# Optimization experiments

Hardware: AMD Instinct MI355X
Metric: run time of the kernel (lower is better)

The kernel has to match this reference:

```python
import jax, jax.numpy as jnp
import numpy as np

INF = 1e20


def setup_inputs() -> dict:
    key = jax.random.key(0)
    k0, k1, k2, k3, k4 = jax.random.split(key, 5)
    B, T, C, D = 4, 8, 512, 256
    P, Ks = 4, 4
    return {
        "context": jax.random.normal(k0, (B, T, C, D), jnp.float32),
        "ctx_mask": jax.random.randint(k1, (B, C), 0, 2).astype(jnp.int32),
        "weight_tensor": jax.random.normal(k2, (P, D), jnp.float32),
        "mean_dis": jax.random.uniform(k3, (Ks, 1), jnp.float32),
        "precision_inv_dis": jax.random.uniform(k4, (Ks, 1), jnp.float32),
        "topk": 10,
        "max_position_distance": 160,
    }


def _forward(context, ctx_mask, weight_tensor, mean_dis, precision_inv_dis, topk, max_position_distance):
    B, T, C, D = context.shape
    Ks = mean_dis.shape[0]
    # attention[b,t,c,e] = mean_p sum_d ctx[b,t,c,d]*relu(W[p,d])*ctx[b,t,e,d]
    # (mean over perspectives commutes with the contraction over d)
    wbar = jnp.mean(jax.nn.relu(weight_tensor), axis=0)  # (D,)
    attention = jnp.einsum('btcd,bted->btce', context * wbar, context)  # (B,T,C,C)

    valid = ctx_mask > 0  # (B,C)
    pair_ok = valid[:, None, :, None] & valid[:, None, None, :]  # (B,1,C,C)
    attention = jnp.where(pair_ok, attention, -INF)

    # spatial Gaussian kernels over |i-j| distances (shared across batch/turn)
    idx = jnp.arange(C)
    pc = jnp.abs(idx[:, None] - idx[None, :]).astype(jnp.float32)
    pc = jnp.minimum(pc, float(max_position_distance)) / float(max_position_distance)  # (C,C)
    mu = mean_dis[:, 0][:, None, None]            # (Ks,1,1)
    prec = precision_inv_dis[:, 0][:, None, None]  # (Ks,1,1)
    spatial = jnp.exp(-0.5 * (pc[None] - mu) ** 2 * prec ** 2)  # (Ks,C,C)

    # kNN sparsification
    knn_val, knn_ind = jax.lax.top_k(attention, topk)  # (B,T,C,K)
    sem = jax.nn.softmax(knn_val, axis=-1)             # semantic weights (B,T,C,K)

    idx5 = jnp.broadcast_to(knn_ind[:, :, None, :, :], (B, T, Ks, C, topk))
    spatial_full = jnp.broadcast_to(spatial[None, None], (B, T, Ks, C, C))
    sp_chosen = jnp.take_along_axis(spatial_full, idx5, axis=-1)  # (B,T,Ks,C,K)
    sp_chosen = sp_chosen / jnp.sum(sp_chosen, axis=-1, keepdims=True)

    attn_chosen = sem[:, :, None, :, :] * sp_chosen  # (B,T,Ks,C,K)

    adj = jnp.zeros((B, T, Ks, C, C), dtype=attn_chosen.dtype)
    adj = adj.at[
        jnp.arange(B)[:, None, None, None, None],
        jnp.arange(T)[None, :, None, None, None],
        jnp.arange(Ks)[None, None, :, None, None],
        jnp.arange(C)[None, None, None, :, None],
        idx5,
    ].set(attn_chosen)
    return adj


def reference(context, ctx_mask, weight_tensor, mean_dis, precision_inv_dis, topk, max_position_distance):
    return _forward(context, ctx_mask, weight_tensor, mean_dis, precision_inv_dis, topk, max_position_distance)
```

## Files before the change

kernel.cpp:

```cpp
#include <hip/hip_runtime.h>
#include <math.h>

#define C_ 512
#define D_ 256
#define KS_ 4
#define TOPK_ 10
#define NEG 1e20f

typedef float v2f __attribute__((ext_vector_type(2)));
typedef float v4f __attribute__((ext_vector_type(4)));

__device__ __forceinline__ int csw2(int g) { return g ^ ((g >> 3) & 1); }

#define ASTR 36
#define ASTR3 68
#define BSTR2 260
#define ABUF3 (16 * ASTR3)
#define BBUF3 (16 * BSTR2)

#define BARRIER_LDS() asm volatile("s_waitcnt lgkmcnt(0)\n\ts_barrier" ::: "memory")

#define PKFMA_LO(ACC, AP, BP) \
    asm("v_pk_fma_f32 %0, %1, %2, %0 op_sel:[0,0,0] op_sel_hi:[0,1,1]" \
        : "+v"(ACC) : "v"(AP), "v"(BP));
#define PKFMA_HI(ACC, AP, BP) \
    asm("v_pk_fma_f32 %0, %1, %2, %0 op_sel:[1,0,0] op_sel_hi:[1,1,1]" \
        : "+v"(ACC) : "v"(AP), "v"(BP));

extern "C" __global__ __launch_bounds__(256, 2)
void gemm_attn(const float* __restrict__ ctx,
               const float* __restrict__ W,
               float* __restrict__ ws,
               float* __restrict__ out)
{
    __shared__ __align__(16) float wbar_s[D_];
    __shared__ __align__(16) float a_s[2 * ABUF3];
    __shared__ __align__(16) float b_s[2 * BBUF3];

    const int tid  = threadIdx.x;
    const int lane = tid & 63;
    const int wv   = tid >> 6;
    const int wr   = (wv >> 1) * 32;
    const int wc   = (wv & 1) * 128;
    const int rg   = lane >> 4;
    const int cg   = lane & 15;

    const int blk  = blockIdx.x;
    const int bt   = (blk & 7) * 4 + ((blk >> 3) & 3);
    const int tile = blk >> 5;
    const int c0   = (tile & 7) * 64;
    const int n0   = (tile >> 3) * 256;

    const float* ctx_bt = ctx + (size_t)bt * (C_ * D_);
    float* zbase = out + (size_t)blk * 65536 + (size_t)tid * 4;

    {
        float w0 = W[tid], w1 = W[D_ + tid], w2 = W[2 * D_ + tid], w3 = W[3 * D_ + tid];
        wbar_s[tid] = 0.25f * (fmaxf(w0, 0.f) + fmaxf(w1, 0.f) + fmaxf(w2, 0.f) + fmaxf(w3, 0.f));
    }

    const int bcol = tid >> 2;
    const int bq   = tid & 3;
    const float* bsrc = ctx_bt + (size_t)(n0 + bcol) * D_ + bq * 4;
    const int bwoff = (4 * bq) * BSTR2 + bcol;
    const int ar_ = tid >> 2;
    const int aq  = tid & 3;
    const float* asrc = ctx_bt + (size_t)(c0 + ar_) * D_ + aq * 4;
    const int awoff = (4 * aq) * ASTR3 + ar_;
    const int abase = wr + rg * 8;
    const int bbase = wc + cg * 4;

    BARRIER_LDS();

    {
        v4f B0 = *(const v4f*)(bsrc + (size_t)0 * 64 * D_);
        v4f B1 = *(const v4f*)(bsrc + (size_t)1 * 64 * D_);
        v4f B2 = *(const v4f*)(bsrc + (size_t)2 * 64 * D_);
        v4f B3 = *(const v4f*)(bsrc + (size_t)3 * 64 * D_);
        v4f A0 = *(const v4f*)asrc;
        #pragma unroll
        for (int j = 0; j < 4; ++j) {
            b_s[bwoff + j * BSTR2 + 0 * 64] = B0[j];
            b_s[bwoff + j * BSTR2 + 1 * 64] = B1[j];
            b_s[bwoff + j * BSTR2 + 2 * 64] = B2[j];
            b_s[bwoff + j * BSTR2 + 3 * 64] = B3[j];
        }
        v4f wb = *(const v4f*)(wbar_s + aq * 4);
        a_s[awoff + 0 * ASTR3] = A0[0] * wb[0];
        a_s[awoff + 1 * ASTR3] = A0[1] * wb[1];
        a_s[awoff + 2 * ASTR3] = A0[2] * wb[2];
        a_s[awoff + 3 * ASTR3] = A0[3] * wb[3];
    }
    BARRIER_LDS();

    v2f acc2[8][4];
    #pragma unroll
    for (int j = 0; j < 8; ++j)
        #pragma unroll
        for (int t = 0; t < 4; ++t) acc2[j][t] = (v2f){0.f, 0.f};

    #define FMA_RANGE(K0, K1)                                                 \
        _Pragma("unroll")                                                     \
        for (int kk = (K0); kk < (K1); ++kk) {                                \
            v4f av0 = *(const v4f*)(acur + kk * ASTR3 + abase);               \
            v4f av1 = *(const v4f*)(acur + kk * ASTR3 + abase + 4);           \
            v4f bv0 = *(const v4f*)(bcur + kk * BSTR2 + bbase);               \
            v4f bv1 = *(const v4f*)(bcur + kk * BSTR2 + bbase + 64);          \
            v2f a01 = __builtin_shufflevector(av0, av0, 0, 1);                \
            v2f a23 = __builtin_shufflevector(av0, av0, 2, 3);                \
            v2f a45 = __builtin_shufflevector(av1, av1, 0, 1);                \
            v2f a67 = __builtin_shufflevector(av1, av1, 2, 3);                \
            v2f b0l = __builtin_shufflevector(bv0, bv0, 0, 1);                \
            v2f b0h = __builtin_shufflevector(bv0, bv0, 2, 3);                \
            v2f b1l = __builtin_shufflevector(bv1, bv1, 0, 1);                \
            v2f b1h = __builtin_shufflevector(bv1, bv1, 2, 3);                \
            PKFMA_LO(acc2[0][0], a01, b0l) PKFMA_LO(acc2[0][1], a01, b0h)     \
            PKFMA_LO(acc2[0][2], a01, b1l) PKFMA_LO(acc2[0][3], a01, b1h)     \
            PKFMA_HI(acc2[1][0], a01, b0l) PKFMA_HI(acc2[1][1], a01, b0h)     \
            PKFMA_HI(acc2[1][2], a01, b1l) PKFMA_HI(acc2[1][3], a01, b1h)     \
            PKFMA_LO(acc2[2][0], a23, b0l) PKFMA_LO(acc2[2][1], a23, b0h)     \
            PKFMA_LO(acc2[2][2], a23, b1l) PKFMA_LO(acc2[2][3], a23, b1h)     \
            PKFMA_HI(acc2[3][0], a23, b0l) PKFMA_HI(acc2[3][1], a23, b0h)     \
            PKFMA_HI(acc2[3][2], a23, b1l) PKFMA_HI(acc2[3][3], a23, b1h)     \
            PKFMA_LO(acc2[4][0], a45, b0l) PKFMA_LO(acc2[4][1], a45, b0h)     \
            PKFMA_LO(acc2[4][2], a45, b1l) PKFMA_LO(acc2[4][3], a45, b1h)     \
            PKFMA_HI(acc2[5][0], a45, b0l) PKFMA_HI(acc2[5][1], a45, b0h)     \
            PKFMA_HI(acc2[5][2], a45, b1l) PKFMA_HI(acc2[5][3], a45, b1h)     \
            PKFMA_LO(acc2[6][0], a67, b0l) PKFMA_LO(acc2[6][1], a67, b0h)     \
            PKFMA_LO(acc2[6][2], a67, b1l) PKFMA_LO(acc2[6][3], a67, b1h)     \
            PKFMA_HI(acc2[7][0], a67, b0l) PKFMA_HI(acc2[7][1], a67, b0h)     \
            PKFMA_HI(acc2[7][2], a67, b1l) PKFMA_HI(acc2[7][3], a67, b1h)     \
        }

    const v4f zv = (v4f){0.f, 0.f, 0.f, 0.f};

    for (int kt = 0; kt < 16; ++kt) {
        const float* acur = a_s + (kt & 1) * ABUF3;
        const float* bcur = b_s + (kt & 1) * BBUF3;
        float* anx = a_s + ((kt & 1) ^ 1) * ABUF3;
        float* bnx = b_s + ((kt & 1) ^ 1) * BBUF3;
        const bool pf = (kt < 15);

        v4f B0, B1, B2, B3, A0;
        if (pf) {
            const float* nb = bsrc + (kt + 1) * 16;
            B0 = *(const v4f*)(nb + (size_t)0 * 64 * D_);
            B1 = *(const v4f*)(nb + (size_t)1 * 64 * D_);
            B2 = *(const v4f*)(nb + (size_t)2 * 64 * D_);
            B3 = *(const v4f*)(nb + (size_t)3 * 64 * D_);
            A0 = *(const v4f*)(asrc + (kt + 1) * 16);
        }
        #pragma unroll
        for (int q = 0; q < 4; ++q)
            *(v4f*)(zbase + (size_t)(kt * 4 + q) * 1024) = zv;

        FMA_RANGE(0, 10)
        if (pf) {
            #pragma unroll
            for (int j = 0; j < 4; ++j) {
                bnx[bwoff + j * BSTR2 + 0 * 64] = B0[j];
                bnx[bwoff + j * BSTR2 + 1 * 64] = B1[j];
                bnx[bwoff + j * BSTR2 + 2 * 64] = B2[j];
                bnx[bwoff + j * BSTR2 + 3 * 64] = B3[j];
            }
            v4f wb = *(const v4f*)(wbar_s + (kt + 1) * 16 + aq * 4);
            anx[awoff + 0 * ASTR3] = A0[0] * wb[0];
            anx[awoff + 1 * ASTR3] = A0[1] * wb[1];
            anx[awoff + 2 * ASTR3] = A0[2] * wb[2];
            anx[awoff + 3 * ASTR3] = A0[3] * wb[3];
        }
        FMA_RANGE(10, 16)
        BARRIER_LDS();
    }
    #undef FMA_RANGE

    #pragma unroll
    for (int j = 0; j < 8; ++j) {
        float* wrow = ws + ((size_t)bt * C_ + c0 + wr + rg * 8 + j) * C_ + n0;
        v4f o0 = __builtin_shufflevector(acc2[j][0], acc2[j][1], 0, 1, 2, 3);
        v4f o1 = __builtin_shufflevector(acc2[j][2], acc2[j][3], 0, 1, 2, 3);
        *(v4f*)(wrow + bbase)      = o0;
        *(v4f*)(wrow + bbase + 64) = o1;
    }
}

extern "C" __global__ __launch_bounds__(256, 2)
void epilogue_k(const float* __restrict__ ws,
                const int* __restrict__ cmask,
                const float* __restrict__ mu_g,
                const float* __restrict__ pr_g,
                float* __restrict__ out)
{
    const int tid  = threadIdx.x;
    const int lane = tid & 63;
    const int wv   = tid >> 6;

    const int blk = blockIdx.x;
    const int bt  = blk >> 7;
    const int rq  = blk & 127;
    const int b   = bt >> 3;

    const int c  = rq * 4 + wv;
    const int vr = cmask[b * C_ + c];

    float row[8];
    {
        const float* wrow = ws + ((size_t)bt * C_ + c) * C_ + lane * 8;
        float4 r0 = *(const float4*)wrow;
        float4 r1 = *(const float4*)(wrow + 4);
        row[0] = r0.x; row[1] = r0.y; row[2] = r0.z; row[3] = r0.w;
        row[4] = r1.x; row[5] = r1.y; row[6] = r1.z; row[7] = r1.w;
        int4 m0 = *(const int4*)(cmask + b * C_ + lane * 8);
        int4 m1 = *(const int4*)(cmask + b * C_ + lane * 8 + 4);
        int em[8] = {m0.x, m0.y, m0.z, m0.w, m1.x, m1.y, m1.z, m1.w};
        #pragma unroll
        for (int i = 0; i < 8; ++i) {
            bool ok = (vr > 0) && (em[i] > 0);
            row[i] = ok ? row[i] : -NEG;
        }
    }

    float tv[TOPK_];
    int   te[TOPK_];
    unsigned int taken = 0;
    #pragma unroll
    for (int j = 0; j < TOPK_; ++j) {
        float lv = -3.3e38f;
        int   li = 0;
        #pragma unroll
        for (int i = 0; i < 8; ++i) {
            bool better = (!((taken >> i) & 1u)) && (row[i] > lv);
            lv = better ? row[i] : lv;
            li = better ? i : li;
        }
        int le = lane * 8 + li;
        #pragma unroll
        for (int off = 1; off < 64; off <<= 1) {
            float ov = __shfl_xor(lv, off);
            int   oe = __shfl_xor(le, off);
            bool take = (ov > lv) || (ov == lv && oe < le);
            lv = take ? ov : lv;
            le = take ? oe : le;
        }
        tv[j] = lv;
        te[j] = le;
        if ((le >> 3) == lane) taken |= 1u << (le & 7);
    }
    const float mx = tv[0];
    float ssum = 0.f;
    #pragma unroll
    for (int j = 0; j < TOPK_; ++j) ssum += expf(tv[j] - mx);

    if (lane < 40) {
        const int ksq = lane / 10;
        const int myj = lane - ksq * 10;
        const float mu = mu_g[ksq];
        const float pr = pr_g[ksq];
        float sps = 0.f, spj = 0.f, tvj = 0.f;
        int ej = 0;
        #pragma unroll
        for (int j = 0; j < TOPK_; ++j) {
            float d = fabsf((float)(te[j] - c));
            d = fminf(d, 160.f) * (1.0f / 160.0f);
            float x  = d - mu;
            float sp = expf(-0.5f * x * x * pr * pr);
            sps += sp;
            if (j == myj) { spj = sp; tvj = tv[j]; ej = te[j]; }
        }
        float oval = (expf(tvj - mx) / ssum) * (spj / sps);
        out[((size_t)(bt * KS_ + ksq) * C_ + c) * C_ + ej] = oval;
    }
}

#define BSTR 516
extern "C" __global__ __launch_bounds__(256, 2)
void graph_learner(const float* __restrict__ ctx,
                   const int* __restrict__ cmask,
                   const float* __restrict__ W,
                   const float* __restrict__ mu_g,
                   const float* __restrict__ pr_g,
                   float* __restrict__ out)
{
    __shared__ __align__(16) float wbar_s[D_];
    __shared__ __align__(16) float a_s[16 * ASTR];
    __shared__ __align__(16) float b_s[16 * BSTR];
    __shared__ __align__(8)  float res_s[2560];
    __shared__ unsigned int vmask_s[16];

    const int tid  = threadIdx.x;
    const int lane = tid & 63;
    const int wv   = tid >> 6;
    const int w8   = wv * 8;

    const int blk = blockIdx.x;
    const int bt  = (blk & 7) * 4 + ((blk >> 3) & 3);
    const int c0  = (blk >> 5) * 32;
    const int b   = bt >> 3;

    const float* ctx_bt = ctx + (size_t)bt * (C_ * D_);
    const int*   mask_b = cmask + b * C_;

    {
        float w0 = W[tid], w1 = W[D_ + tid], w2 = W[2 * D_ + tid], w3 = W[3 * D_ + tid];
        wbar_s[tid] = 0.25f * (fmaxf(w0, 0.f) + fmaxf(w1, 0.f) + fmaxf(w2, 0.f) + fmaxf(w3, 0.f));
    }
    if (tid < 16) {
        unsigned int m = 0;
        for (int i = 0; i < 32; ++i)
            m |= (mask_b[tid * 32 + i] > 0 ? 1u : 0u) << i;
        vmask_s[tid] = m;
    }

    const int brow = tid >> 2;
    const int bq   = tid & 3;
    const float* bsrc = ctx_bt + (size_t)brow * D_ + bq * 4;
    const int bwbase = (4 * bq) * BSTR + 4 * csw2(brow >> 2) + (brow & 3);
    const int ar_ = tid >> 2;
    const int aq  = tid & 3;
    const float* asrc = ctx_bt + (size_t)(c0 + ar_) * D_ + aq * 4;
    const int awbase = (4 * aq) * ASTR + ar_;
    const int bc0 = 4 * csw2(2 * lane);
    const int bc1 = 4 * csw2(2 * lane + 1);

    v2f acc2[8][4];
    #pragma unroll
    for (int j = 0; j < 8; ++j)
        #pragma unroll
        for (int t = 0; t < 4; ++t) acc2[j][t] = (v2f){0.f, 0.f};

    for (int kt = 0; kt < 16; ++kt) {
        __syncthreads();
        #pragma unroll
        for (int i = 0; i < 8; ++i) {
            float4 v = *(const float4*)(bsrc + (size_t)i * 64 * D_ + kt * 16);
            b_s[bwbase + 0 * BSTR + i * 64] = v.x;
            b_s[bwbase + 1 * BSTR + i * 64] = v.y;
            b_s[bwbase + 2 * BSTR + i * 64] = v.z;
            b_s[bwbase + 3 * BSTR + i * 64] = v.w;
        }
        if (tid < 128) {
            float4 v  = *(const float4*)(asrc + kt * 16);
            float4 wb = *(const float4*)(wbar_s + kt * 16 + aq * 4);
            a_s[awbase + 0 * ASTR] = v.x * wb.x;
            a_s[awbase + 1 * ASTR] = v.y * wb.y;
            a_s[awbase + 2 * ASTR] = v.z * wb.z;
            a_s[awbase + 3 * ASTR] = v.w * wb.w;
        }
        __syncthreads();
        #pragma unroll
        for (int kk = 0; kk < 16; ++kk) {
            float4 av0 = *(const float4*)(a_s + kk * ASTR + w8);
            float4 av1 = *(const float4*)(a_s + kk * ASTR + w8 + 4);
            float4 bv0 = *(const float4*)(b_s + kk * BSTR + bc0);
            float4 bv1 = *(const float4*)(b_s + kk * BSTR + bc1);
            v2f b20 = (v2f){bv0.x, bv0.y};
            v2f b21 = (v2f){bv0.z, bv0.w};
            v2f b22 = (v2f){bv1.x, bv1.y};
            v2f b23 = (v2f){bv1.z, bv1.w};
            float ar8[8] = {av0.x, av0.y, av0.z, av0.w, av1.x, av1.y, av1.z, av1.w};
            #pragma unroll
            for (int j = 0; j < 8; ++j) {
                v2f a2 = (v2f){ar8[j], ar8[j]};
                asm("v_pk_fma_f32 %0, %1, %2, %0" : "+v"(acc2[j][0]) : "v"(a2), "v"(b20));
                asm("v_pk_fma_f32 %0, %1, %2, %0" : "+v"(acc2[j][1]) : "v"(a2), "v"(b21));
                asm("v_pk_fma_f32 %0, %1, %2, %0" : "+v"(acc2[j][2]) : "v"(a2), "v"(b22));
                asm("v_pk_fma_f32 %0, %1, %2, %0" : "+v"(acc2[j][3]) : "v"(a2), "v"(b23));
            }
        }
    }

    {
        const float4 z = make_float4(0.f, 0.f, 0.f, 0.f);
        #pragma unroll
        for (int ks = 0; ks < KS_; ++ks) {
            float* ob = out + ((size_t)(bt * KS_ + ks) * C_ + c0) * C_;
            #pragma unroll
            for (int i = 0; i < 16; ++i)
                *(float4*)(ob + (size_t)(tid + i * 256) * 4) = z;
        }
    }

    const unsigned int em8 = (vmask_s[lane >> 2] >> ((lane & 3) * 8)) & 0xffu;
    const float mu0 = mu_g[0], mu1 = mu_g[1], mu2 = mu_g[2], mu3 = mu_g[3];
    const float pr0 = pr_g[0], pr1 = pr_g[1], pr2 = pr_g[2], pr3 = pr_g[3];

    #pragma unroll
    for (int jr = 0; jr < 8; ++jr) {
        const int c  = c0 + w8 + jr;
        const int vr = mask_b[c];
        float row[8];
        #pragma unroll
        for (int t = 0; t < 4; ++t) { row[2 * t] = acc2[jr][t].x; row[2 * t + 1] = acc2[jr][t].y; }
        #pragma unroll
        for (int i = 0; i < 8; ++i) {
            bool ok = (vr > 0) && ((em8 >> i) & 1u);
            row[i] = ok ? row[i] : -NEG;
        }
        float tv[TOPK_];
        int   te[TOPK_];
        unsigned int taken = 0;
        #pragma unroll
        for (int j = 0; j < TOPK_; ++j) {
            float lv = -3.3e38f;
            int   li = 0;
            #pragma unroll
            for (int i = 0; i < 8; ++i) {
                bool better = (!((taken >> i) & 1u)) && (row[i] > lv);
                lv = better ? row[i] : lv;
                li = better ? i : li;
            }
            int le = lane * 8 + li;
            #pragma unroll
            for (int off = 1; off < 64; off <<= 1) {
                float ov = __shfl_xor(lv, off);
                int   oe = __shfl_xor(le, off);
                bool take = (ov > lv) || (ov == lv && oe < le);
                lv = take ? ov : lv;
                le = take ? oe : le;
            }
            tv[j] = lv;
            te[j] = le;
            if ((le >> 3) == lane) taken |= 1u << (le & 7);
        }
        const float mx = tv[0];
        float ssum = 0.f;
        #pragma unroll
        for (int j = 0; j < TOPK_; ++j) ssum += expf(tv[j] - mx);

        if (lane < 40) {
            const int ksq = lane / 10;
            const int myj = lane - ksq * 10;
            const float mu = (ksq == 0) ? mu0 : (ksq == 1) ? mu1 : (ksq == 2) ? mu2 : mu3;
            const float pr = (ksq == 0) ? pr0 : (ksq == 1) ? pr1 : (ksq == 2) ? pr2 : pr3;
            float sps = 0.f, spj = 0.f, tvj = 0.f;
            int ej = 0;
            #pragma unroll
            for (int j = 0; j < TOPK_; ++j) {
                float d = fabsf((float)(te[j] - c));
                d = fminf(d, 160.f) * (1.0f / 160.0f);
                float x  = d - mu;
                float sp = expf(-0.5f * x * x * pr * pr);
                sps += sp;
                if (j == myj) { spj = sp; tvj = tv[j]; ej = te[j]; }
            }
            float val = (expf(tvj - mx) / ssum) * (spj / sps);
            int   off = ((bt * KS_ + ksq) * C_ + c) * C_ + ej;
            int   slot = (((wv * 8 + jr) * 40) + lane) * 2;
            res_s[slot]     = val;
            res_s[slot + 1] = __int_as_float(off);
        }
    }

    __syncthreads();
    #pragma unroll
    for (int i = 0; i < 5; ++i) {
        int p = tid * 5 + i;
        float v   = res_s[2 * p];
        int   off = __float_as_int(res_s[2 * p + 1]);
        out[off] = v;
    }
}

extern "C" void kernel_launch(void* const* d_in, const int* in_sizes, int n_in,
                              void* d_out, int out_size, void* d_ws, size_t ws_size,
                              hipStream_t stream) {
    (void)in_sizes; (void)n_in; (void)out_size;
    const float* ctx   = (const float*)d_in[0];
    const int*   cmask = (const int*)d_in[1];
    const float* W     = (const float*)d_in[2];
    const float* mu    = (const float*)d_in[3];
    const float* pr    = (const float*)d_in[4];
    const size_t WS_NEEDED = (size_t)32 * C_ * C_ * sizeof(float);
    if (ws_size >= WS_NEEDED) {
        float* ws = (float*)d_ws;
        gemm_attn<<<dim3(512), dim3(256), 0, stream>>>(ctx, W, ws, (float*)d_out);
        epilogue_k<<<dim3(4096), dim3(256), 0, stream>>>(ws, cmask, mu, pr, (float*)d_out);
    } else {
        graph_learner<<<dim3(512), dim3(256), 0, stream>>>(ctx, cmask, W, mu, pr, (float*)d_out);
    }
}
```

Measured before the change: 95.08 us.

## Write full dense output rows in epilogue instead of zero-filling in GEMM

Removes the zero-fill of the whole output that the GEMM kernel interleaved with its main loop. The epilogue now writes each complete output row per kernel itself: each lane builds four-float vectors holding either zero or the selected top-k weight and stores them with nontemporal vector stores. The output is then written once instead of zeroed and scattered again, but the epilogue does more store work and the GEMM loses the overlap of zero-filling with compute.

```diff
diff --git a/kernel.cpp b/kernel.cpp
--- a/kernel.cpp
+++ b/kernel.cpp
@@ -30,8 +30,7 @@
 extern "C" __global__ __launch_bounds__(256, 2)
 void gemm_attn(const float* __restrict__ ctx,
                const float* __restrict__ W,
-               float* __restrict__ ws,
-               float* __restrict__ out)
+               float* __restrict__ ws)
 {
     __shared__ __align__(16) float wbar_s[D_];
     __shared__ __align__(16) float a_s[2 * ABUF3];
@@ -52,7 +51,6 @@
     const int n0   = (tile >> 3) * 256;
 
     const float* ctx_bt = ctx + (size_t)bt * (C_ * D_);
-    float* zbase = out + (size_t)blk * 65536 + (size_t)tid * 4;
 
     {
         float w0 = W[tid], w1 = W[D_ + tid], w2 = W[2 * D_ + tid], w3 = W[3 * D_ + tid];
@@ -132,8 +130,6 @@
             PKFMA_HI(acc2[7][2], a67, b1l) PKFMA_HI(acc2[7][3], a67, b1h)     \
         }
 
-    const v4f zv = (v4f){0.f, 0.f, 0.f, 0.f};
-
     for (int kt = 0; kt < 16; ++kt) {
         const float* acur = a_s + (kt & 1) * ABUF3;
         const float* bcur = b_s + (kt & 1) * BBUF3;
@@ -150,10 +146,6 @@
             B3 = *(const v4f*)(nb + (size_t)3 * 64 * D_);
             A0 = *(const v4f*)(asrc + (kt + 1) * 16);
         }
-        #pragma unroll
-        for (int q = 0; q < 4; ++q)
-            *(v4f*)(zbase + (size_t)(kt * 4 + q) * 1024) = zv;
-
         FMA_RANGE(0, 10)
         if (pf) {
             #pragma unroll
@@ -251,13 +243,13 @@
     #pragma unroll
     for (int j = 0; j < TOPK_; ++j) ssum += expf(tv[j] - mx);
 
-    if (lane < 40) {
-        const int ksq = lane / 10;
-        const int myj = lane - ksq * 10;
+    float wval;
+    {
+        const int ksq = (lane < 40) ? (lane / 10) : 3;
+        const int myj = (lane < 40) ? (lane - (lane / 10) * 10) : 0;
         const float mu = mu_g[ksq];
         const float pr = pr_g[ksq];
         float sps = 0.f, spj = 0.f, tvj = 0.f;
-        int ej = 0;
         #pragma unroll
         for (int j = 0; j < TOPK_; ++j) {
             float d = fabsf((float)(te[j] - c));
@@ -265,10 +257,42 @@
             float x  = d - mu;
             float sp = expf(-0.5f * x * x * pr * pr);
             sps += sp;
-            if (j == myj) { spj = sp; tvj = tv[j]; ej = te[j]; }
-        }
-        float oval = (expf(tvj - mx) / ssum) * (spj / sps);
-        out[((size_t)(bt * KS_ + ksq) * C_ + c) * C_ + ej] = oval;
+            if (j == myj) { spj = sp; tvj = tv[j]; }
+        }
+        wval = (expf(tvj - mx) / ssum) * (spj / sps);
+    }
+
+    const int base1 = lane * 4;
+    const int base2 = 256 + lane * 4;
+    bool m1[TOPK_][4], m2[TOPK_][4];
+    #pragma unroll
+    for (int j = 0; j < TOPK_; ++j) {
+        int ej = te[j];
+        #pragma unroll
+        for (int e = 0; e < 4; ++e) {
+            m1[j][e] = (ej == base1 + e);
+            m2[j][e] = (ej == base2 + e);
+        }
+    }
+
+    #pragma unroll
+    for (int ksq = 0; ksq < KS_; ++ksq) {
+        float r1[4] = {0.f, 0.f, 0.f, 0.f};
+        float r2[4] = {0.f, 0.f, 0.f, 0.f};
+        #pragma unroll
+        for (int j = 0; j < TOPK_; ++j) {
+            float wj = __shfl(wval, ksq * 10 + j);
+            #pragma unroll
+            for (int e = 0; e < 4; ++e) {
+                r1[e] = m1[j][e] ? wj : r1[e];
+                r2[e] = m2[j][e] ? wj : r2[e];
+            }
+        }
+        float* orow = out + ((size_t)(bt * KS_ + ksq) * C_ + c) * C_;
+        v4f o1 = (v4f){r1[0], r1[1], r1[2], r1[3]};
+        v4f o2 = (v4f){r2[0], r2[1], r2[2], r2[3]};
+        __builtin_nontemporal_store(o1, (v4f*)(orow + base1));
+        __builtin_nontemporal_store(o2, (v4f*)(orow + base2));
     }
 }
 
@@ -473,7 +497,7 @@
     const size_t WS_NEEDED = (size_t)32 * C_ * C_ * sizeof(float);
     if (ws_size >= WS_NEEDED) {
         float* ws = (float*)d_ws;
-        gemm_attn<<<dim3(512), dim3(256), 0, stream>>>(ctx, W, ws, (float*)d_out);
+        gemm_attn<<<dim3(512), dim3(256), 0, stream>>>(ctx, W, ws);
         epilogue_k<<<dim3(4096), dim3(256), 0, stream>>>(ws, cmask, mu, pr, (float*)d_out);
     } else {
         graph_learner<<<dim3(512), dim3(256), 0, stream>>>(ctx, cmask, W, mu, pr, (float*)d_out);
```

Measured after the change: 102.0 us. +7.3%, slower.
